# Kernel tuning notes

Hardware: AMD Instinct MI355X
Metric: run time of the kernel (lower is better)

The kernel has to match this reference:

```python
import jax, jax.numpy as jnp
import numpy as np

N = 100_000      # total nodes in batched graph
NE = 800_000     # total edges
G = 1_000        # number of graphs in batch
V_DIM = 128      # node feat dim (== H_DIM, required by GRUCell usage)
E_DIM = 64       # edge feat dim
H_DIM = 128      # hidden dim
K_HEAD = 4       # multi-scale interaction heads


def _leaky(x):
    return jnp.where(x >= 0, x, 0.1 * x)


def _gru_cell(x, h, Wih, Whh, bih, bhh):
    # torch nn.GRUCell math; Wih/Whh stored as [in, 3*h] with (r,z,n) chunk order
    gi = x @ Wih + bih
    gh = h @ Whh + bhh
    ir, iz, inn = jnp.split(gi, 3, axis=-1)
    hr, hz, hn = jnp.split(gh, 3, axis=-1)
    r = jax.nn.sigmoid(ir + hr)
    z = jax.nn.sigmoid(iz + hz)
    n = jnp.tanh(inn + r * hn)
    return (1.0 - z) * n + z * h


def setup_inputs() -> dict:
    key = jax.random.key(0)
    ks = iter(jax.random.split(key, 48))
    def rn(shape, scale=0.05):
        return (jax.random.normal(next(ks), shape) * scale).astype(jnp.float32)
    inp = {}
    inp["v"] = rn((N, V_DIM), 1.0)
    inp["e"] = rn((NE, E_DIM), 1.0)
    inp["s"] = rn((G, V_DIM), 1.0)
    inp["edge_src"] = jax.random.randint(next(ks), (NE,), 0, N)
    inp["edge_dst"] = jax.random.randint(next(ks), (NE,), 0, N)
    inp["node_graph"] = jnp.repeat(jnp.arange(G), N // G)  # sorted segment ids
    # top-level linears (stored [in, out])
    inp["A_w"] = rn((V_DIM, H_DIM)); inp["A_b"] = rn((H_DIM,))
    inp["mA_w"] = rn((K_HEAD, V_DIM, H_DIM)); inp["mA_b"] = rn((K_HEAD, H_DIM))
    inp["mB_w"] = rn((K_HEAD, V_DIM, H_DIM)); inp["mB_b"] = rn((K_HEAD, H_DIM))
    inp["mC_w"] = rn((K_HEAD, H_DIM)); inp["mC_b"] = rn((K_HEAD,))
    inp["mD_w"] = rn((K_HEAD, V_DIM, H_DIM)); inp["mD_b"] = rn((K_HEAD, H_DIM))
    inp["B_w"] = rn((H_DIM * K_HEAD, H_DIM)); inp["B_b"] = rn((H_DIM,))
    inp["C_w"] = rn((V_DIM, H_DIM)); inp["C_b"] = rn((H_DIM,))
    inp["K_w"] = rn((E_DIM, H_DIM)); inp["K_b"] = rn((H_DIM,))
    inp["E_w"] = rn((H_DIM + V_DIM, H_DIM)); inp["E_b"] = rn((H_DIM,))
    for pfx in ("gm", "gs"):
        inp[pfx + "_A_w"] = rn((H_DIM, H_DIM)); inp[pfx + "_A_b"] = rn((H_DIM,))
        inp[pfx + "_B_w"] = rn((H_DIM, H_DIM)); inp[pfx + "_B_b"] = rn((H_DIM,))
        inp[pfx + "_Wih"] = rn((H_DIM, 3 * H_DIM)); inp[pfx + "_Whh"] = rn((H_DIM, 3 * H_DIM))
        inp[pfx + "_bih"] = rn((3 * H_DIM,)); inp[pfx + "_bhh"] = rn((3 * H_DIM,))
    return inp


def reference(v, e, s, edge_src, edge_dst, node_graph,
              A_w, A_b, mA_w, mA_b, mB_w, mB_b, mC_w, mC_b, mD_w, mD_b,
              B_w, B_b, C_w, C_b, K_w, K_b, E_w, E_b,
              gm_A_w, gm_A_b, gm_B_w, gm_B_b, gm_Wih, gm_Whh, gm_bih, gm_bhh,
              gs_A_w, gs_A_b, gs_B_w, gs_B_b, gs_Wih, gs_Whh, gs_bih, gs_bhh):
    # super -> super
    s2s = jnp.tanh(s @ A_w + A_b)                                       # [G,H]
    # multi-head node->super attention pooling (Multi_scale_interaction)
    d_node = jnp.tanh(jnp.einsum('nv,kvh->knh', v, mA_w) + mA_b[:, None, :])     # [K,N,H]
    d_super = jnp.tanh(jnp.einsum('gv,kvh->kgh', s, mB_w) + mB_b[:, None, :])    # [K,G,H]
    a = jnp.einsum('knh,kh->nk', d_node * d_super[:, node_graph, :], mC_w) + mC_b[None, :]  # [N,K]
    a_max = jax.ops.segment_max(a, node_graph, num_segments=G, indices_are_sorted=True)
    a_exp = jnp.exp(a - a_max[node_graph])
    denom = jax.ops.segment_sum(a_exp, node_graph, num_segments=G, indices_are_sorted=True)
    attn = a_exp / denom[node_graph]                                    # per-graph softmax, [N,K]
    d_v = jnp.einsum('nv,kvh->nkh', v, mD_w) + mD_b[None, :, :]         # [N,K,H]
    pooled = jax.ops.segment_sum(d_v * attn[:, :, None], node_graph, num_segments=G,
                                 indices_are_sorted=True)               # [G,K,H]
    m2s = jnp.tanh(pooled.reshape(G, K_HEAD * H_DIM) @ B_w + B_b)       # [G,H]
    # super -> node broadcast
    s2m = jnp.tanh(s @ C_w + C_b)[node_graph]                           # [N,H]
    # edge-wise message: leaky_relu(K(e) * v_src) summed into destination node
    ve = _leaky((e @ K_w + K_b) * v[edge_src])                          # [E,H]
    sve = jax.ops.segment_sum(ve, edge_dst, num_segments=N)             # [N,H]
    m2m = _leaky(jnp.concatenate([sve, v], axis=1) @ E_w + E_b)         # [N,H]
    # adaptive GRU gate: node update
    z_m = jax.nn.sigmoid(m2m @ gm_A_w + gm_A_b + s2m @ gm_B_w + gm_B_b)
    h_m = z_m * s2m + (1.0 - z_m) * m2m
    update_v = _gru_cell(v, h_m, gm_Wih, gm_Whh, gm_bih, gm_bhh)
    # adaptive GRU gate: supernode update
    z_s = jax.nn.sigmoid(s2s @ gs_A_w + gs_A_b + m2s @ gs_B_w + gs_B_b)
    h_s = z_s * m2s + (1.0 - z_s) * s2s
    update_s = _gru_cell(s, h_s, gs_Wih, gs_Whh, gs_bih, gs_bhh)
    return (update_v, update_s)
```

## Files before the change

kernel.cpp:

```cpp
#include <hip/hip_runtime.h>

#define NN   100000
#define NEDG 800000
#define NG   1000
#define HD   128
#define EDIM 64

#define NB3 (NEDG / 64)
#define NB2 ((NN + 63) / 64)
#define NB6 ((NN + 63) / 64)
#define NB4 (NN / 32)
#define W0B 108
#define MH_HIST 3125
#define Z_F4 3200000
#define Z_TOT 3300000
#define ZB ((Z_TOT + 255) / 256)
#define M0_GRID (W0B + NG + ZB)

typedef unsigned short u16;
typedef __bf16 bf16x8 __attribute__((ext_vector_type(8)));
typedef float f32x4 __attribute__((ext_vector_type(4)));
typedef u16 u16x8 __attribute__((ext_vector_type(8)));
typedef unsigned u32x4 __attribute__((ext_vector_type(4)));

#define MFMA16(a, b, c) __builtin_amdgcn_mfma_f32_16x16x32_bf16(a, b, c, 0, 0, 0)

#define WS_E    0
#define WS_GA   4096
#define WS_WIH  6144
#define WS_WHH  12288
#define WS_MA0  18432
#define WS_KW   26624
#define WS_LANES 27648

#define BF(base, NTT, ks, nt, lane) \
    (*(const bf16x8*)(wsw + (size_t)((base) + (((ks) * (NTT) + (nt)) * 64 + (lane))) * 8))

__device__ __forceinline__ float sigmoidf_(float x) { return 1.0f / (1.0f + __expf(-x)); }
__device__ __forceinline__ float tanhf_(float x) {
    float ax = fabsf(x);
    float e  = __expf(-2.0f * ax);
    float t  = (1.0f - e) / (1.0f + e);
    return copysignf(t, x);
}
__device__ __forceinline__ float leaky_(float x) { return x >= 0.f ? x : 0.1f * x; }
__device__ __forceinline__ u16 f2bf(float x) {
    union { float f; unsigned u; } c; c.f = x;
    unsigned r = c.u + 0x7FFF + ((c.u >> 16) & 1);
    return (u16)(r >> 16);
}
__device__ __forceinline__ float bfbits2f(unsigned hw) {
    union { unsigned u; float f; } c; c.u = hw << 16; return c.f;
}
__device__ __forceinline__ unsigned pack2bf(float lo, float hi) {
    return (unsigned)f2bf(lo) | ((unsigned)f2bf(hi) << 16);
}
__device__ __forceinline__ bf16x8 mk8(const float* __restrict__ p) {
    float4 a = *(const float4*)p;
    float4 b = *(const float4*)(p + 4);
    union { u32x4 u; bf16x8 v; } c;
    c.u[0] = pack2bf(a.x, a.y);
    c.u[1] = pack2bf(a.z, a.w);
    c.u[2] = pack2bf(b.x, b.y);
    c.u[3] = pack2bf(b.z, b.w);
    return c.v;
}

__device__ __forceinline__ void stg1(u16* lds, int P, int r, int c, u16 val) {
    int byteoff = (c << 1) ^ ((r & 7) << 4);
    lds[r * P + (byteoff >> 1)] = val;
}
__device__ __forceinline__ bf16x8 ldA(const u16* lds, int P, int r, int ks, int hi) {
    int byteoff = (ks * 64 + (hi << 4)) ^ ((r & 7) << 4);
    return *(const bf16x8*)(lds + r * P + (byteoff >> 1));
}

__device__ __forceinline__ void wconv_body(
    int t,
    const float* __restrict__ E_w, const float* __restrict__ gmA_w,
    const float* __restrict__ Wih, const float* __restrict__ Whh,
    const float* __restrict__ mA_w, const float* __restrict__ K_w,
    u16* __restrict__ dst)
{
    const float* W; int N; int local;
    if (t < 4096)       { W = E_w;  N = 128; local = t; }
    else if (t < 6144)  { W = gmA_w; N = 128; local = t - 4096; }
    else if (t < 12288) { W = Wih;  N = 384; local = t - 6144; }
    else if (t < 18432) { W = Whh;  N = 384; local = t - 12288; }
    else if (t < 26624) { int k = (t - 18432) >> 11; W = mA_w + k * 128 * 128; N = 128; local = (t - 18432) & 2047; }
    else                { W = K_w;  N = 128; local = t - 26624; }
    int lane = local & 63;
    int fid  = local >> 6;
    int NT = N >> 4;
    int ks = fid / NT, nt = fid - ks * NT;
    int krow = ks * 32 + ((lane >> 4) << 3);
    int col  = nt * 16 + (lane & 15);
    u16* d = dst + (size_t)t * 8;
    #pragma unroll
    for (int j = 0; j < 8; j++) d[j] = f2bf(W[(size_t)(krow + j) * N + col]);
}

__device__ __forceinline__ void k1_body(
    int g, int t,
    const float* __restrict__ s,
    const float* __restrict__ A_w, const float* __restrict__ A_b,
    const float* __restrict__ mB_w, const float* __restrict__ mB_b,
    const float* __restrict__ mC_w,
    const float* __restrict__ C_w, const float* __restrict__ C_b,
    const float* __restrict__ gmB_w, const float* __restrict__ gmA_b, const float* __restrict__ gmB_b,
    float* __restrict__ s2s, float* __restrict__ wkg,
    float* __restrict__ s2m_tab, float* __restrict__ t2,
    float* __restrict__ vbar, float* __restrict__ denom)
{
    __shared__ float sm[HD];
    __shared__ float sm2[HD];
    if (t < HD) sm[t] = s[g * HD + t];
    else {
        int i = t - 128;
        #pragma unroll
        for (int j = 0; j < 4; j++) vbar[(size_t)g * 512 + i + 128 * j] = 0.f;
        if (i < 4) denom[g * 4 + i] = 0.f;
    }
    __syncthreads();
    float s2m = 0.f;
    if (t < HD) {
        {
            float a = 0.f;
            #pragma unroll 8
            for (int i = 0; i < HD; i++) a = fmaf(sm[i], A_w[i * HD + t], a);
            s2s[g * HD + t] = tanhf_(a + A_b[t]);
        }
        for (int k = 0; k < 4; k++) {
            float a = 0.f;
            const float* W = mB_w + k * HD * HD;
            #pragma unroll 8
            for (int i = 0; i < HD; i++) a = fmaf(sm[i], W[i * HD + t], a);
            float d = tanhf_(a + mB_b[k * HD + t]);
            wkg[(k * NG + g) * HD + t] = d * mC_w[k * HD + t];
        }
        {
            float a = 0.f;
            #pragma unroll 8
            for (int i = 0; i < HD; i++) a = fmaf(sm[i], C_w[i * HD + t], a);
            s2m = tanhf_(a + C_b[t]);
            s2m_tab[g * HD + t] = s2m;
            sm2[t] = s2m;
        }
    }
    __syncthreads();
    if (t < HD) {
        float a = 0.f;
        #pragma unroll 8
        for (int i = 0; i < HD; i++) a = fmaf(sm2[i], gmB_w[i * HD + t], a);
        t2[g * HD + t] = a + gmA_b[t] + gmB_b[t];
    }
}

__global__ __launch_bounds__(256) void mega0(
    const float* __restrict__ E_w, const float* __restrict__ gmA_w,
    const float* __restrict__ Wih, const float* __restrict__ Whh,
    const float* __restrict__ mA_w, const float* __restrict__ K_w,
    u16* __restrict__ wswz,
    const float* __restrict__ s,
    const float* __restrict__ A_w, const float* __restrict__ A_b,
    const float* __restrict__ mB_w, const float* __restrict__ mB_b,
    const float* __restrict__ mC_w,
    const float* __restrict__ C_w, const float* __restrict__ C_b,
    const float* __restrict__ gmB_w, const float* __restrict__ gmA_b, const float* __restrict__ gmB_b,
    float* __restrict__ s2s, float* __restrict__ wkg,
    float* __restrict__ s2m_tab, float* __restrict__ t2,
    float* __restrict__ vbar, float* __restrict__ denom,
    float* __restrict__ sve, int* __restrict__ cnt)
{
    const int bid = blockIdx.x, tid = threadIdx.x;
    if (bid < W0B) {
        wconv_body(bid * 256 + tid, E_w, gmA_w, Wih, Whh, mA_w, K_w, wswz);
    } else if (bid < W0B + NG) {
        k1_body(bid - W0B, tid, s, A_w, A_b, mB_w, mB_b, mC_w, C_w, C_b,
                gmB_w, gmA_b, gmB_b, s2s, wkg, s2m_tab, t2, vbar, denom);
    } else {
        long idx = (long)(bid - W0B - NG) * 256 + tid;
        if (idx < Z_F4) ((float4*)sve)[idx] = make_float4(0.f, 0.f, 0.f, 0.f);
        else if (idx < Z_TOT) cnt[idx - Z_F4] = 0;
    }
}

__device__ __forceinline__ void k2_body(
    int bid, int tid,
    const float* __restrict__ v, const int* __restrict__ ngr,
    const u16* __restrict__ wsw,
    const float* __restrict__ mA_b, const float* __restrict__ mC_b,
    const float* __restrict__ wkg,
    float* __restrict__ aexp, float* __restrict__ denom)
{
    const int lane = tid & 63, w = tid >> 6;
    const int l15 = lane & 15, hi = lane >> 4;
    const int n0 = bid * 64 + w * 16;
    const int arow = min(n0 + l15, NN - 1);
    bf16x8 av[4];
    #pragma unroll
    for (int ks = 0; ks < 4; ks++)
        av[ks] = mk8(v + (size_t)arow * HD + ks * 32 + hi * 8);
    int gq[4], nodeq[4];
    #pragma unroll
    for (int q = 0; q < 4; q++) {
        int nd = n0 + hi * 4 + q;
        nodeq[q] = nd;
        gq[q] = ngr[min(nd, NN - 1)];
    }
    for (int k = 0; k < 4; k++) {
        float rs[4] = {0.f, 0.f, 0.f, 0.f};
        const float* bias = mA_b + k * HD;
        #pragma unroll
        for (int nt = 0; nt < 8; nt++) {
            f32x4 acc = {0.f, 0.f, 0.f, 0.f};
            #pragma unroll
            for (int ks = 0; ks < 4; ks++)
                acc = MFMA16(av[ks], BF(WS_MA0 + k * 2048, 8, ks, nt, lane), acc);
            int col = nt * 16 + l15;
            float bb = bias[col];
            #pragma unroll
            for (int q = 0; q < 4; q++)
                rs[q] += tanhf_(acc[q] + bb) * wkg[((size_t)k * NG + gq[q]) * HD + col];
        }
        #pragma unroll
        for (int q = 0; q < 4; q++) {
            float x = rs[q];
            x += __shfl_xor(x, 1); x += __shfl_xor(x, 2);
            x += __shfl_xor(x, 4); x += __shfl_xor(x, 8);
            if (l15 == 0 && nodeq[q] < NN) {
                float ev = __expf(x + mC_b[k]);
                aexp[(size_t)nodeq[q] * 4 + k] = ev;
                atomicAdd(&denom[gq[q] * 4 + k], ev);
            }
        }
    }
}

__global__ __launch_bounds__(256) void megaH(
    const int* __restrict__ edst, int* __restrict__ cnt,
    const float* __restrict__ v, const int* __restrict__ ngr,
    const u16* __restrict__ wsw,
    const float* __restrict__ mA_b, const float* __restrict__ mC_b,
    const float* __restrict__ wkg,
    float* __restrict__ aexp, float* __restrict__ denom)
{
    const int bid = blockIdx.x, tid = threadIdx.x;
    if (bid < MH_HIST) {
        int i = bid * 256 + tid;
        if (i < NEDG) atomicAdd(&cnt[edst[i]], 1);
    } else {
        k2_body(bid - MH_HIST, tid, v, ngr, wsw, mA_b, mC_b, wkg, aexp, denom);
    }
}

__global__ __launch_bounds__(256) void k_scan1(const int* __restrict__ cnt,
                                               int* __restrict__ excl, int* __restrict__ bsum) {
    __shared__ int sd[256];
    int t = threadIdx.x, b = blockIdx.x;
    int base = b * 1024 + t * 4;
    int v0 = (base + 0 < NN) ? cnt[base + 0] : 0;
    int v1 = (base + 1 < NN) ? cnt[base + 1] : 0;
    int v2 = (base + 2 < NN) ? cnt[base + 2] : 0;
    int v3 = (base + 3 < NN) ? cnt[base + 3] : 0;
    int s = v0 + v1 + v2 + v3;
    sd[t] = s;
    __syncthreads();
    for (int off = 1; off < 256; off <<= 1) {
        int x = (t >= off) ? sd[t - off] : 0;
        __syncthreads();
        sd[t] += x;
        __syncthreads();
    }
    int incl = sd[t];
    int ex = incl - s;
    if (base + 0 < NN) excl[base + 0] = ex;
    if (base + 1 < NN) excl[base + 1] = ex + v0;
    if (base + 2 < NN) excl[base + 2] = ex + v0 + v1;
    if (base + 3 < NN) excl[base + 3] = ex + v0 + v1 + v2;
    if (t == 255) bsum[b] = incl;
}

#define NSCB 98
__global__ void k_scan2(int* __restrict__ bsum) {
    if (threadIdx.x == 0 && blockIdx.x == 0) {
        int run = 0;
        for (int i = 0; i < NSCB; i++) { int t = bsum[i]; bsum[i] = run; run += t; }
    }
}

__global__ __launch_bounds__(256) void k_scatter_fused(
    const int* __restrict__ edst,
    const int* __restrict__ excl, const int* __restrict__ bsum,
    int* __restrict__ cnt, int* __restrict__ perm)
{
    int i = blockIdx.x * 256 + threadIdx.x;
    if (i < NEDG) {
        int d = edst[i];
        int rank = atomicSub(&cnt[d], 1) - 1;
        perm[excl[d] + bsum[d >> 10] + rank] = i;
    }
}

#define OPW 66
__global__ __launch_bounds__(256) void k3_merge(
    const float* __restrict__ e, const float* __restrict__ v,
    const int* __restrict__ esrc, const int* __restrict__ edst,
    const int* __restrict__ perm,
    const u16* __restrict__ wsw, const float* __restrict__ K_b,
    float* __restrict__ sve)
{
    __shared__ unsigned OUTP[64 * OPW];
    __shared__ int pid[64];
    __shared__ int dsta[64];
    const int tid = threadIdx.x;
    const int e0 = blockIdx.x * 64;
    if (tid < 64) {
        int p = perm[e0 + tid];
        pid[tid] = p;
        dsta[tid] = edst[p];
    }
    const int lane = tid & 63, w = tid >> 6;
    const int l15 = lane & 15, hi = lane >> 4;
    const int rbase = w * 16;
    const int myrow = perm[e0 + rbase + l15];
    bf16x8 ae[2];
    #pragma unroll
    for (int ks = 0; ks < 2; ks++)
        ae[ks] = mk8(e + (size_t)myrow * EDIM + ks * 32 + hi * 8);
    __syncthreads();
    int sq[4];
    #pragma unroll
    for (int q = 0; q < 4; q++) sq[q] = esrc[pid[rbase + hi * 4 + q]];
    u16* OU = (u16*)OUTP;
    #pragma unroll
    for (int nt = 0; nt < 8; nt++) {
        f32x4 acc = {0.f, 0.f, 0.f, 0.f};
        acc = MFMA16(ae[0], BF(WS_KW, 8, 0, nt, lane), acc);
        acc = MFMA16(ae[1], BF(WS_KW, 8, 1, nt, lane), acc);
        int col = nt * 16 + l15;
        float kb = K_b[col];
        #pragma unroll
        for (int q = 0; q < 4; q++) {
            float val = leaky_((acc[q] + kb) * v[(size_t)sq[q] * HD + col]);
            OU[(rbase + hi * 4 + q) * (OPW * 2) + col] = f2bf(val);
        }
    }
    __syncthreads();
    {
        const int cp = tid & 63;
        const int qr = tid >> 6;
        const int r0 = qr * 16;
        int dcur = dsta[r0];
        unsigned x = OUTP[r0 * OPW + cp];
        float a0 = bfbits2f(x & 0xffff), a1 = bfbits2f(x >> 16);
        #pragma unroll
        for (int i = 1; i < 16; i++) {
            int r = r0 + i;
            int d = dsta[r];
            unsigned y = OUTP[r * OPW + cp];
            float y0 = bfbits2f(y & 0xffff), y1 = bfbits2f(y >> 16);
            if (d == dcur) { a0 += y0; a1 += y1; }
            else {
                atomicAdd(&sve[(size_t)dcur * HD + cp * 2 + 0], a0);
                atomicAdd(&sve[(size_t)dcur * HD + cp * 2 + 1], a1);
                dcur = d; a0 = y0; a1 = y1;
            }
        }
        atomicAdd(&sve[(size_t)dcur * HD + cp * 2 + 0], a0);
        atomicAdd(&sve[(size_t)dcur * HD + cp * 2 + 1], a1);
    }
}

__global__ __launch_bounds__(256) void k3_edge_unsorted(
    const float* __restrict__ e, const float* __restrict__ v,
    const int* __restrict__ esrc, const int* __restrict__ edst,
    const u16* __restrict__ wsw, const float* __restrict__ K_b,
    float* __restrict__ sve)
{
    const int tid = threadIdx.x;
    const int e0 = blockIdx.x * 64;
    const int lane = tid & 63, w = tid >> 6;
    const int l15 = lane & 15, hi = lane >> 4;
    const int rbase = w * 16;
    const int myrow = e0 + rbase + l15;
    bf16x8 ae[2];
    #pragma unroll
    for (int ks = 0; ks < 2; ks++)
        ae[ks] = mk8(e + (size_t)myrow * EDIM + ks * 32 + hi * 8);
    int sq[4], dq[4];
    #pragma unroll
    for (int q = 0; q < 4; q++) {
        int ei = e0 + rbase + hi * 4 + q;
        sq[q] = esrc[ei]; dq[q] = edst[ei];
    }
    #pragma unroll
    for (int nt = 0; nt < 8; nt++) {
        f32x4 acc = {0.f, 0.f, 0.f, 0.f};
        acc = MFMA16(ae[0], BF(WS_KW, 8, 0, nt, lane), acc);
        acc = MFMA16(ae[1], BF(WS_KW, 8, 1, nt, lane), acc);
        int col = nt * 16 + l15;
        float kb = K_b[col];
        #pragma unroll
        for (int q = 0; q < 4; q++) {
            float val = leaky_((acc[q] + kb) * v[(size_t)sq[q] * HD + col]);
            atomicAdd(&sve[(size_t)dq[q] * HD + col], val);
        }
    }
}

__device__ __forceinline__ void k4_body(
    int bid, int tid,
    const float* __restrict__ v, const int* __restrict__ ngr,
    const float* __restrict__ aexp, const float* __restrict__ denom,
    float* __restrict__ vbar)
{
    const int d = tid & 127;
    const int hf = tid >> 7;
    const int n0 = bid * 32 + hf * 16;
    int gcur = -1;
    float a0 = 0.f, a1 = 0.f, a2 = 0.f, a3 = 0.f;
    float4 rd = make_float4(0.f, 0.f, 0.f, 0.f);
    for (int nd = 0; nd < 16; nd++) {
        int n = n0 + nd;
        int g = ngr[n];
        if (g != gcur) {
            if (gcur >= 0) {
                atomicAdd(&vbar[(gcur * 4 + 0) * HD + d], a0);
                atomicAdd(&vbar[(gcur * 4 + 1) * HD + d], a1);
                atomicAdd(&vbar[(gcur * 4 + 2) * HD + d], a2);
                atomicAdd(&vbar[(gcur * 4 + 3) * HD + d], a3);
                a0 = a1 = a2 = a3 = 0.f;
            }
            float4 dn = *(const float4*)&denom[g * 4];
            rd = make_float4(1.f / dn.x, 1.f / dn.y, 1.f / dn.z, 1.f / dn.w);
            gcur = g;
        }
        float4 ae = *(const float4*)&aexp[n * 4];
        float vv = v[(size_t)n * HD + d];
        a0 = fmaf(ae.x * rd.x, vv, a0);
        a1 = fmaf(ae.y * rd.y, vv, a1);
        a2 = fmaf(ae.z * rd.z, vv, a2);
        a3 = fmaf(ae.w * rd.w, vv, a3);
    }
    atomicAdd(&vbar[(gcur * 4 + 0) * HD + d], a0);
    atomicAdd(&vbar[(gcur * 4 + 1) * HD + d], a1);
    atomicAdd(&vbar[(gcur * 4 + 2) * HD + d], a2);
    atomicAdd(&vbar[(gcur * 4 + 3) * HD + d], a3);
}

__device__ __forceinline__ void k6_body(
    int bid, int tid, u16* T,
    const float* __restrict__ v, const int* __restrict__ ngr,
    const float* __restrict__ sve, const u16* __restrict__ wsw,
    const float* __restrict__ E_b,
    const float* __restrict__ s2m_tab, const float* __restrict__ t2,
    const float* __restrict__ bih, const float* __restrict__ bhh,
    float* __restrict__ out_v)
{
    const int lane = tid & 63;
    const int l15 = lane & 15, hi = lane >> 4;
    const int n0 = bid * 64 + (tid >> 6) * 16;
    const int arow = min(n0 + l15, NN - 1);
    bf16x8 av[4], ax[4];
    #pragma unroll
    for (int ks = 0; ks < 4; ks++) {
        av[ks] = mk8(v   + (size_t)arow * HD + ks * 32 + hi * 8);
        ax[ks] = mk8(sve + (size_t)arow * HD + ks * 32 + hi * 8);
    }
    int gq[4], nodeq[4];
    #pragma unroll
    for (int q = 0; q < 4; q++) {
        int nd = n0 + hi * 4 + q;
        nodeq[q] = nd;
        gq[q] = ngr[min(nd, NN - 1)];
    }
    unsigned m2mp[8][2];
    #pragma unroll
    for (int nt = 0; nt < 8; nt++) {
        f32x4 acc = {0.f, 0.f, 0.f, 0.f};
        #pragma unroll
        for (int ks = 0; ks < 4; ks++) acc = MFMA16(ax[ks], BF(WS_E, 8, ks, nt, lane), acc);
        #pragma unroll
        for (int ks = 0; ks < 4; ks++) acc = MFMA16(av[ks], BF(WS_E, 8, 4 + ks, nt, lane), acc);
        float eb = E_b[nt * 16 + l15];
        float m0 = leaky_(acc[0] + eb), m1 = leaky_(acc[1] + eb);
        float m2 = leaky_(acc[2] + eb), m3 = leaky_(acc[3] + eb);
        m2mp[nt][0] = pack2bf(m0, m1);
        m2mp[nt][1] = pack2bf(m2, m3);
        int col = nt * 16 + l15;
        stg1(T, 128, hi * 4 + 0, col, (u16)(m2mp[nt][0] & 0xffff));
        stg1(T, 128, hi * 4 + 1, col, (u16)(m2mp[nt][0] >> 16));
        stg1(T, 128, hi * 4 + 2, col, (u16)(m2mp[nt][1] & 0xffff));
        stg1(T, 128, hi * 4 + 3, col, (u16)(m2mp[nt][1] >> 16));
    }
    bf16x8 am[4];
    #pragma unroll
    for (int ks = 0; ks < 4; ks++) am[ks] = ldA(T, 128, l15, ks, hi);
    unsigned hmp[8][2];
    #pragma unroll
    for (int nt = 0; nt < 8; nt++) {
        f32x4 acc = {0.f, 0.f, 0.f, 0.f};
        #pragma unroll
        for (int ks = 0; ks < 4; ks++) acc = MFMA16(am[ks], BF(WS_GA, 8, ks, nt, lane), acc);
        int col = nt * 16 + l15;
        float m2mq[4] = { bfbits2f(m2mp[nt][0] & 0xffff), bfbits2f(m2mp[nt][0] >> 16),
                          bfbits2f(m2mp[nt][1] & 0xffff), bfbits2f(m2mp[nt][1] >> 16) };
        float hm[4];
        #pragma unroll
        for (int q = 0; q < 4; q++) {
            int g = gq[q];
            float z = sigmoidf_(acc[q] + t2[(size_t)g * HD + col]);
            hm[q] = z * s2m_tab[(size_t)g * HD + col] + (1.f - z) * m2mq[q];
        }
        hmp[nt][0] = pack2bf(hm[0], hm[1]);
        hmp[nt][1] = pack2bf(hm[2], hm[3]);
        stg1(T, 128, hi * 4 + 0, col, (u16)(hmp[nt][0] & 0xffff));
        stg1(T, 128, hi * 4 + 1, col, (u16)(hmp[nt][0] >> 16));
        stg1(T, 128, hi * 4 + 2, col, (u16)(hmp[nt][1] & 0xffff));
        stg1(T, 128, hi * 4 + 3, col, (u16)(hmp[nt][1] >> 16));
    }
    bf16x8 ah[4];
    #pragma unroll
    for (int ks = 0; ks < 4; ks++) ah[ks] = ldA(T, 128, l15, ks, hi);
    #pragma unroll
    for (int nt = 0; nt < 8; nt++) {
        f32x4 air = {0.f,0.f,0.f,0.f}, aiz = {0.f,0.f,0.f,0.f}, ain = {0.f,0.f,0.f,0.f};
        f32x4 ahr = {0.f,0.f,0.f,0.f}, ahz = {0.f,0.f,0.f,0.f}, ahn = {0.f,0.f,0.f,0.f};
        #pragma unroll
        for (int ks = 0; ks < 4; ks++) {
            air = MFMA16(av[ks], BF(WS_WIH, 24, ks, nt,      lane), air);
            ahr = MFMA16(ah[ks], BF(WS_WHH, 24, ks, nt,      lane), ahr);
            aiz = MFMA16(av[ks], BF(WS_WIH, 24, ks, nt + 8,  lane), aiz);
            ahz = MFMA16(ah[ks], BF(WS_WHH, 24, ks, nt + 8,  lane), ahz);
            ain = MFMA16(av[ks], BF(WS_WIH, 24, ks, nt + 16, lane), ain);
            ahn = MFMA16(ah[ks], BF(WS_WHH, 24, ks, nt + 16, lane), ahn);
        }
        int col = nt * 16 + l15;
        float br  = bih[col] + bhh[col];
        float bz  = bih[HD + col] + bhh[HD + col];
        float bi3 = bih[2 * HD + col];
        float bh3 = bhh[2 * HD + col];
        float hmq[4] = { bfbits2f(hmp[nt][0] & 0xffff), bfbits2f(hmp[nt][0] >> 16),
                         bfbits2f(hmp[nt][1] & 0xffff), bfbits2f(hmp[nt][1] >> 16) };
        #pragma unroll
        for (int q = 0; q < 4; q++) {
            float r   = sigmoidf_(air[q] + ahr[q] + br);
            float z   = sigmoidf_(aiz[q] + ahz[q] + bz);
            float nnv = tanhf_(ain[q] + bi3 + r * (ahn[q] + bh3));
            if (nodeq[q] < NN)
                out_v[(size_t)nodeq[q] * HD + col] = (1.f - z) * nnv + z * hmq[q];
        }
    }
}

__global__ __launch_bounds__(256) void mega2(
    const float* __restrict__ v, const int* __restrict__ ngr,
    const float* __restrict__ sve, const u16* __restrict__ wsw,
    const float* __restrict__ E_b,
    const float* __restrict__ s2m_tab, const float* __restrict__ t2,
    const float* __restrict__ bih, const float* __restrict__ bhh,
    const float* __restrict__ aexp, const float* __restrict__ denom,
    float* __restrict__ out_v, float* __restrict__ vbar)
{
    __shared__ u16 TT[4][16 * 128];
    const int bid = blockIdx.x, tid = threadIdx.x;
    if (bid < NB6) {
        k6_body(bid, tid, TT[tid >> 6], v, ngr, sve, wsw, E_b, s2m_tab, t2, bih, bhh, out_v);
    } else {
        k4_body(bid - NB6, tid, v, ngr, aexp, denom, vbar);
    }
}

__global__ __launch_bounds__(128) void k5_super(
    const float* __restrict__ s, const float* __restrict__ vbar,
    const float* __restrict__ mD_w, const float* __restrict__ mD_b,
    const float* __restrict__ B_w, const float* __restrict__ B_b,
    const float* __restrict__ s2s,
    const float* __restrict__ gsA_w, const float* __restrict__ gsA_b,
    const float* __restrict__ gsB_w, const float* __restrict__ gsB_b,
    const float* __restrict__ gsWih, const float* __restrict__ gsWhh,
    const float* __restrict__ gsbih, const float* __restrict__ gsbhh,
    float* __restrict__ out_s)
{
    __shared__ float vb[4 * HD];
    __shared__ float p[4 * HD];
    __shared__ float m2s_l[HD];
    __shared__ float s2s_l[HD];
    __shared__ float hs_l[HD];
    __shared__ float srow[HD];
    const int g = blockIdx.x, t = threadIdx.x;
    #pragma unroll
    for (int l = 0; l < 4; l++) vb[t + HD * l] = vbar[(size_t)g * 4 * HD + t + HD * l];
    srow[t]  = s[g * HD + t];
    s2s_l[t] = s2s[g * HD + t];
    __syncthreads();
    for (int k = 0; k < 4; k++) {
        float a = 0.f;
        const float* W = mD_w + k * HD * HD;
        #pragma unroll 8
        for (int i = 0; i < HD; i++) a = fmaf(vb[k * HD + i], W[i * HD + t], a);
        p[k * HD + t] = a + mD_b[k * HD + t];
    }
    __syncthreads();
    float m2s;
    {
        float a = 0.f;
        #pragma unroll 8
        for (int j = 0; j < 4 * HD; j++) a = fmaf(p[j], B_w[j * HD + t], a);
        m2s = tanhf_(a + B_b[t]);
        m2s_l[t] = m2s;
    }
    __syncthreads();
    float hs;
    {
        float za = 0.f, zb = 0.f;
        #pragma unroll 8
        for (int i = 0; i < HD; i++) {
            za = fmaf(s2s_l[i], gsA_w[i * HD + t], za);
            zb = fmaf(m2s_l[i], gsB_w[i * HD + t], zb);
        }
        float z = sigmoidf_(za + gsA_b[t] + zb + gsB_b[t]);
        hs = z * m2s + (1.f - z) * s2s_l[t];
        hs_l[t] = hs;
    }
    __syncthreads();
    float gi0 = 0.f, gh0 = 0.f, gi1 = 0.f, gh1 = 0.f, gi2 = 0.f, gh2 = 0.f;
    #pragma unroll 4
    for (int i = 0; i < HD; i++) {
        float sv = srow[i], hv = hs_l[i];
        gi0 = fmaf(sv, gsWih[i * 384 + t], gi0);
        gh0 = fmaf(hv, gsWhh[i * 384 + t], gh0);
        gi1 = fmaf(sv, gsWih[i * 384 + 128 + t], gi1);
        gh1 = fmaf(hv, gsWhh[i * 384 + 128 + t], gh1);
        gi2 = fmaf(sv, gsWih[i * 384 + 256 + t], gi2);
        gh2 = fmaf(hv, gsWhh[i * 384 + 256 + t], gh2);
    }
    float r  = sigmoidf_(gi0 + gsbih[t] + gh0 + gsbhh[t]);
    float z2 = sigmoidf_(gi1 + gsbih[128 + t] + gh1 + gsbhh[128 + t]);
    float nn = tanhf_(gi2 + gsbih[256 + t] + r * (gh2 + gsbhh[256 + t]));
    out_s[g * HD + t] = (1.f - z2) * nn + z2 * hs;
}

extern "C" void kernel_launch(void* const* d_in, const int* in_sizes, int n_in,
                              void* d_out, int out_size, void* d_ws, size_t ws_size,
                              hipStream_t stream)
{
    const float* v    = (const float*)d_in[0];
    const float* e    = (const float*)d_in[1];
    const float* s    = (const float*)d_in[2];
    const int*   esrc = (const int*)d_in[3];
    const int*   edst = (const int*)d_in[4];
    const int*   ngr  = (const int*)d_in[5];
    const float* A_w  = (const float*)d_in[6];
    const float* A_b  = (const float*)d_in[7];
    const float* mA_w = (const float*)d_in[8];
    const float* mA_b = (const float*)d_in[9];
    const float* mB_w = (const float*)d_in[10];
    const float* mB_b = (const float*)d_in[11];
    const float* mC_w = (const float*)d_in[12];
    const float* mC_b = (const float*)d_in[13];
    const float* mD_w = (const float*)d_in[14];
    const float* mD_b = (const float*)d_in[15];
    const float* B_w  = (const float*)d_in[16];
    const float* B_b  = (const float*)d_in[17];
    const float* C_w  = (const float*)d_in[18];
    const float* C_b  = (const float*)d_in[19];
    const float* K_w  = (const float*)d_in[20];
    const float* K_b  = (const float*)d_in[21];
    const float* E_w  = (const float*)d_in[22];
    const float* E_b  = (const float*)d_in[23];
    const float* gmA_w = (const float*)d_in[24];
    const float* gmA_b = (const float*)d_in[25];
    const float* gmB_w = (const float*)d_in[26];
    const float* gmB_b = (const float*)d_in[27];
    const float* gmWih = (const float*)d_in[28];
    const float* gmWhh = (const float*)d_in[29];
    const float* gmbih = (const float*)d_in[30];
    const float* gmbhh = (const float*)d_in[31];
    const float* gsA_w = (const float*)d_in[32];
    const float* gsA_b = (const float*)d_in[33];
    const float* gsB_w = (const float*)d_in[34];
    const float* gsB_b = (const float*)d_in[35];
    const float* gsWih = (const float*)d_in[36];
    const float* gsWhh = (const float*)d_in[37];
    const float* gsbih = (const float*)d_in[38];
    const float* gsbhh = (const float*)d_in[39];

    float* ws      = (float*)d_ws;
    float* sve     = ws;
    float* aexp    = sve + 12800000;
    float* denom   = aexp + 400000;
    float* wkg     = denom + 4000;
    float* s2s     = wkg + 512000;
    float* s2m_tab = s2s + 128000;
    float* t2      = s2m_tab + 128000;
    float* vbar    = t2 + 128000;
    u16*   wswz    = (u16*)(vbar + 512000);
    int*   isc     = (int*)(wswz + 221184);
    int*   cnt     = isc;
    int*   excl    = cnt + 100000;
    int*   bsum    = excl + 100000;
    int*   startp  = bsum + 128;
    int*   perm    = startp + 100000;
    const size_t NEED_SORT = ((size_t)(perm + 800000 - (int*)d_ws)) * 4;
    const bool do_sort = ws_size >= NEED_SORT;

    float* out_v = (float*)d_out;
    float* out_s = out_v + (size_t)NN * HD;

    mega0<<<M0_GRID, 256, 0, stream>>>(E_w, gmA_w, gmWih, gmWhh, mA_w, K_w, wswz,
                                       s, A_w, A_b, mB_w, mB_b, mC_w, C_w, C_b,
                                       gmB_w, gmA_b, gmB_b, s2s, wkg, s2m_tab, t2,
                                       vbar, denom, sve, cnt);
    megaH<<<MH_HIST + NB2, 256, 0, stream>>>(edst, cnt, v, ngr, wswz, mA_b, mC_b,
                                             wkg, aexp, denom);
    if (do_sort) {
        k_scan1<<<NSCB, 256, 0, stream>>>(cnt, excl, bsum);
        k_scan2<<<1, 64, 0, stream>>>(bsum);
        k_scatter_fused<<<(NEDG + 255) / 256, 256, 0, stream>>>(edst, excl, bsum, cnt, perm);
        k3_merge<<<NB3, 256, 0, stream>>>(e, v, esrc, edst, perm, wswz, K_b, sve);
    } else {
        k3_edge_unsorted<<<NEDG / 64, 256, 0, stream>>>(e, v, esrc, edst, wswz, K_b, sve);
    }
    mega2<<<NB6 + NB4, 256, 0, stream>>>(v, ngr, sve, wswz, E_b, s2m_tab, t2,
                                         gmbih, gmbhh, aexp, denom, out_v, vbar);
    k5_super<<<NG, 128, 0, stream>>>(s, vbar, mD_w, mD_b, B_w, B_b, s2s,
                                     gsA_w, gsA_b, gsB_w, gsB_b,
                                     gsWih, gsWhh, gsbih, gsbhh, out_s);
}
```

Before: 679.7 us.

## Fuse scan passes, co-launch node pooling with edge kernel, merge super update into node kernel

Merges the two scan kernels into one, using an atomic ticket so the last block does the block-sum prefix. Moves the per-graph pooling (k4) out of the node-update kernel and into the same launch as the sorted edge kernel. Folds the supernode GRU kernel into the node-update launch as extra blocks. This removes several launches and lets independent work overlap. The costs are a global-atomic last-block pattern that relies on threadfences, and k5 blocks that now run at 256 threads with half of them idle.

```diff
diff --git a/kernel.cpp b/kernel.cpp
--- a/kernel.cpp
+++ b/kernel.cpp
@@ -13,9 +13,10 @@
 #define W0B 108
 #define MH_HIST 3125
 #define Z_F4 3200000
-#define Z_TOT 3300000
-#define ZB ((Z_TOT + 255) / 256)
+#define Z_EXTRA 100001
+#define ZB ((Z_F4 + Z_EXTRA + 255) / 256)
 #define M0_GRID (W0B + NG + ZB)
+#define NSCB 98
 
 typedef unsigned short u16;
 typedef __bf16 bf16x8 __attribute__((ext_vector_type(8)));
@@ -170,7 +171,7 @@
     float* __restrict__ s2s, float* __restrict__ wkg,
     float* __restrict__ s2m_tab, float* __restrict__ t2,
     float* __restrict__ vbar, float* __restrict__ denom,
-    float* __restrict__ sve, int* __restrict__ cnt)
+    float* __restrict__ sve, int* __restrict__ cnt, int* __restrict__ tick)
 {
     const int bid = blockIdx.x, tid = threadIdx.x;
     if (bid < W0B) {
@@ -181,7 +182,11 @@
     } else {
         long idx = (long)(bid - W0B - NG) * 256 + tid;
         if (idx < Z_F4) ((float4*)sve)[idx] = make_float4(0.f, 0.f, 0.f, 0.f);
-        else if (idx < Z_TOT) cnt[idx - Z_F4] = 0;
+        else {
+            long j = idx - Z_F4;
+            if (j < 100000) cnt[j] = 0;
+            else if (j == 100000) tick[0] = 0;
+        }
     }
 }
 
@@ -254,9 +259,12 @@
     }
 }
 
-__global__ __launch_bounds__(256) void k_scan1(const int* __restrict__ cnt,
-                                               int* __restrict__ excl, int* __restrict__ bsum) {
+__global__ __launch_bounds__(256) void k_scan12(
+    const int* __restrict__ cnt,
+    int* __restrict__ excl, int* __restrict__ bsum, int* __restrict__ tick)
+{
     __shared__ int sd[256];
+    __shared__ int amlast;
     int t = threadIdx.x, b = blockIdx.x;
     int base = b * 1024 + t * 4;
     int v0 = (base + 0 < NN) ? cnt[base + 0] : 0;
@@ -279,13 +287,14 @@
     if (base + 2 < NN) excl[base + 2] = ex + v0 + v1;
     if (base + 3 < NN) excl[base + 3] = ex + v0 + v1 + v2;
     if (t == 255) bsum[b] = incl;
-}
-
-#define NSCB 98
-__global__ void k_scan2(int* __restrict__ bsum) {
-    if (threadIdx.x == 0 && blockIdx.x == 0) {
+    __threadfence();
+    if (t == 0) amlast = (atomicAdd(tick, 1) == NSCB - 1) ? 1 : 0;
+    __syncthreads();
+    if (t == 0 && amlast) {
+        __threadfence();
         int run = 0;
-        for (int i = 0; i < NSCB; i++) { int t = bsum[i]; bsum[i] = run; run += t; }
+        for (int i = 0; i < NSCB; i++) { int tv = bsum[i]; bsum[i] = run; run += tv; }
+        __threadfence();
     }
 }
 
@@ -303,18 +312,18 @@
 }
 
 #define OPW 66
-__global__ __launch_bounds__(256) void k3_merge(
+__device__ __forceinline__ void k3_body(
+    int bid, int tid, char* SM,
     const float* __restrict__ e, const float* __restrict__ v,
     const int* __restrict__ esrc, const int* __restrict__ edst,
     const int* __restrict__ perm,
     const u16* __restrict__ wsw, const float* __restrict__ K_b,
     float* __restrict__ sve)
 {
-    __shared__ unsigned OUTP[64 * OPW];
-    __shared__ int pid[64];
-    __shared__ int dsta[64];
-    const int tid = threadIdx.x;
-    const int e0 = blockIdx.x * 64;
+    unsigned* OUTP = (unsigned*)SM;
+    int* pid  = (int*)(SM + 16896);
+    int* dsta = pid + 64;
+    const int e0 = bid * 64;
     if (tid < 64) {
         int p = perm[e0 + tid];
         pid[tid] = p;
@@ -369,43 +378,6 @@
         }
         atomicAdd(&sve[(size_t)dcur * HD + cp * 2 + 0], a0);
         atomicAdd(&sve[(size_t)dcur * HD + cp * 2 + 1], a1);
-    }
-}
-
-__global__ __launch_bounds__(256) void k3_edge_unsorted(
-    const float* __restrict__ e, const float* __restrict__ v,
-    const int* __restrict__ esrc, const int* __restrict__ edst,
-    const u16* __restrict__ wsw, const float* __restrict__ K_b,
-    float* __restrict__ sve)
-{
-    const int tid = threadIdx.x;
-    const int e0 = blockIdx.x * 64;
-    const int lane = tid & 63, w = tid >> 6;
-    const int l15 = lane & 15, hi = lane >> 4;
-    const int rbase = w * 16;
-    const int myrow = e0 + rbase + l15;
-    bf16x8 ae[2];
-    #pragma unroll
-    for (int ks = 0; ks < 2; ks++)
-        ae[ks] = mk8(e + (size_t)myrow * EDIM + ks * 32 + hi * 8);
-    int sq[4], dq[4];
-    #pragma unroll
-    for (int q = 0; q < 4; q++) {
-        int ei = e0 + rbase + hi * 4 + q;
-        sq[q] = esrc[ei]; dq[q] = edst[ei];
-    }
-    #pragma unroll
-    for (int nt = 0; nt < 8; nt++) {
-        f32x4 acc = {0.f, 0.f, 0.f, 0.f};
-        acc = MFMA16(ae[0], BF(WS_KW, 8, 0, nt, lane), acc);
-        acc = MFMA16(ae[1], BF(WS_KW, 8, 1, nt, lane), acc);
-        int col = nt * 16 + l15;
-        float kb = K_b[col];
-        #pragma unroll
-        for (int q = 0; q < 4; q++) {
-            float val = leaky_((acc[q] + kb) * v[(size_t)sq[q] * HD + col]);
-            atomicAdd(&sve[(size_t)dq[q] * HD + col], val);
-        }
     }
 }
 
@@ -449,6 +421,70 @@
     atomicAdd(&vbar[(gcur * 4 + 3) * HD + d], a3);
 }
 
+__global__ __launch_bounds__(256) void mega3(
+    const float* __restrict__ e, const float* __restrict__ v,
+    const int* __restrict__ esrc, const int* __restrict__ edst,
+    const int* __restrict__ perm,
+    const u16* __restrict__ wsw, const float* __restrict__ K_b,
+    float* __restrict__ sve,
+    const int* __restrict__ ngr,
+    const float* __restrict__ aexp, const float* __restrict__ denom,
+    float* __restrict__ vbar)
+{
+    __shared__ __align__(16) char SM[17408];
+    const int bid = blockIdx.x, tid = threadIdx.x;
+    if (bid < NB3) {
+        k3_body(bid, tid, SM, e, v, esrc, edst, perm, wsw, K_b, sve);
+    } else {
+        k4_body(bid - NB3, tid, v, ngr, aexp, denom, vbar);
+    }
+}
+
+__global__ __launch_bounds__(256) void k3_edge_unsorted(
+    const float* __restrict__ e, const float* __restrict__ v,
+    const int* __restrict__ esrc, const int* __restrict__ edst,
+    const u16* __restrict__ wsw, const float* __restrict__ K_b,
+    float* __restrict__ sve)
+{
+    const int tid = threadIdx.x;
+    const int e0 = blockIdx.x * 64;
+    const int lane = tid & 63, w = tid >> 6;
+    const int l15 = lane & 15, hi = lane >> 4;
+    const int rbase = w * 16;
+    const int myrow = e0 + rbase + l15;
+    bf16x8 ae[2];
+    #pragma unroll
+    for (int ks = 0; ks < 2; ks++)
+        ae[ks] = mk8(e + (size_t)myrow * EDIM + ks * 32 + hi * 8);
+    int sq[4], dq[4];
+    #pragma unroll
+    for (int q = 0; q < 4; q++) {
+        int ei = e0 + rbase + hi * 4 + q;
+        sq[q] = esrc[ei]; dq[q] = edst[ei];
+    }
+    #pragma unroll
+    for (int nt = 0; nt < 8; nt++) {
+        f32x4 acc = {0.f, 0.f, 0.f, 0.f};
+        acc = MFMA16(ae[0], BF(WS_KW, 8, 0, nt, lane), acc);
+        acc = MFMA16(ae[1], BF(WS_KW, 8, 1, nt, lane), acc);
+        int col = nt * 16 + l15;
+        float kb = K_b[col];
+        #pragma unroll
+        for (int q = 0; q < 4; q++) {
+            float val = leaky_((acc[q] + kb) * v[(size_t)sq[q] * HD + col]);
+            atomicAdd(&sve[(size_t)dq[q] * HD + col], val);
+        }
+    }
+}
+
+__global__ __launch_bounds__(256) void k4_standalone(
+    const float* __restrict__ v, const int* __restrict__ ngr,
+    const float* __restrict__ aexp, const float* __restrict__ denom,
+    float* __restrict__ vbar)
+{
+    k4_body(blockIdx.x, threadIdx.x, v, ngr, aexp, denom, vbar);
+}
+
 __device__ __forceinline__ void k6_body(
     int bid, int tid, u16* T,
     const float* __restrict__ v, const int* __restrict__ ngr,
@@ -554,25 +590,8 @@
     }
 }
 
-__global__ __launch_bounds__(256) void mega2(
-    const float* __restrict__ v, const int* __restrict__ ngr,
-    const float* __restrict__ sve, const u16* __restrict__ wsw,
-    const float* __restrict__ E_b,
-    const float* __restrict__ s2m_tab, const float* __restrict__ t2,
-    const float* __restrict__ bih, const float* __restrict__ bhh,
-    const float* __restrict__ aexp, const float* __restrict__ denom,
-    float* __restrict__ out_v, float* __restrict__ vbar)
-{
-    __shared__ u16 TT[4][16 * 128];
-    const int bid = blockIdx.x, tid = threadIdx.x;
-    if (bid < NB6) {
-        k6_body(bid, tid, TT[tid >> 6], v, ngr, sve, wsw, E_b, s2m_tab, t2, bih, bhh, out_v);
-    } else {
-        k4_body(bid - NB6, tid, v, ngr, aexp, denom, vbar);
-    }
-}
-
-__global__ __launch_bounds__(128) void k5_super(
+__device__ __forceinline__ void k5_body(
+    int g, int t, float* SM,
     const float* __restrict__ s, const float* __restrict__ vbar,
     const float* __restrict__ mD_w, const float* __restrict__ mD_b,
     const float* __restrict__ B_w, const float* __restrict__ B_b,
@@ -583,28 +602,32 @@
     const float* __restrict__ gsbih, const float* __restrict__ gsbhh,
     float* __restrict__ out_s)
 {
-    __shared__ float vb[4 * HD];
-    __shared__ float p[4 * HD];
-    __shared__ float m2s_l[HD];
-    __shared__ float s2s_l[HD];
-    __shared__ float hs_l[HD];
-    __shared__ float srow[HD];
-    const int g = blockIdx.x, t = threadIdx.x;
-    #pragma unroll
-    for (int l = 0; l < 4; l++) vb[t + HD * l] = vbar[(size_t)g * 4 * HD + t + HD * l];
-    srow[t]  = s[g * HD + t];
-    s2s_l[t] = s2s[g * HD + t];
-    __syncthreads();
-    for (int k = 0; k < 4; k++) {
-        float a = 0.f;
-        const float* W = mD_w + k * HD * HD;
-        #pragma unroll 8
-        for (int i = 0; i < HD; i++) a = fmaf(vb[k * HD + i], W[i * HD + t], a);
-        p[k * HD + t] = a + mD_b[k * HD + t];
-    }
-    __syncthreads();
-    float m2s;
-    {
+    float* vb    = SM;
+    float* p     = SM + 512;
+    float* m2s_l = SM + 1024;
+    float* s2s_l = SM + 1152;
+    float* hs_l  = SM + 1280;
+    float* srow  = SM + 1408;
+    const bool act = t < HD;
+    if (act) {
+        #pragma unroll
+        for (int l = 0; l < 4; l++) vb[t + HD * l] = vbar[(size_t)g * 4 * HD + t + HD * l];
+        srow[t]  = s[g * HD + t];
+        s2s_l[t] = s2s[g * HD + t];
+    }
+    __syncthreads();
+    if (act) {
+        for (int k = 0; k < 4; k++) {
+            float a = 0.f;
+            const float* W = mD_w + k * HD * HD;
+            #pragma unroll 8
+            for (int i = 0; i < HD; i++) a = fmaf(vb[k * HD + i], W[i * HD + t], a);
+            p[k * HD + t] = a + mD_b[k * HD + t];
+        }
+    }
+    __syncthreads();
+    float m2s = 0.f;
+    if (act) {
         float a = 0.f;
         #pragma unroll 8
         for (int j = 0; j < 4 * HD; j++) a = fmaf(p[j], B_w[j * HD + t], a);
@@ -612,8 +635,8 @@
         m2s_l[t] = m2s;
     }
     __syncthreads();
-    float hs;
-    {
+    float hs = 0.f;
+    if (act) {
         float za = 0.f, zb = 0.f;
         #pragma unroll 8
         for (int i = 0; i < HD; i++) {
@@ -625,21 +648,51 @@
         hs_l[t] = hs;
     }
     __syncthreads();
-    float gi0 = 0.f, gh0 = 0.f, gi1 = 0.f, gh1 = 0.f, gi2 = 0.f, gh2 = 0.f;
-    #pragma unroll 4
-    for (int i = 0; i < HD; i++) {
-        float sv = srow[i], hv = hs_l[i];
-        gi0 = fmaf(sv, gsWih[i * 384 + t], gi0);
-        gh0 = fmaf(hv, gsWhh[i * 384 + t], gh0);
-        gi1 = fmaf(sv, gsWih[i * 384 + 128 + t], gi1);
-        gh1 = fmaf(hv, gsWhh[i * 384 + 128 + t], gh1);
-        gi2 = fmaf(sv, gsWih[i * 384 + 256 + t], gi2);
-        gh2 = fmaf(hv, gsWhh[i * 384 + 256 + t], gh2);
-    }
-    float r  = sigmoidf_(gi0 + gsbih[t] + gh0 + gsbhh[t]);
-    float z2 = sigmoidf_(gi1 + gsbih[128 + t] + gh1 + gsbhh[128 + t]);
-    float nn = tanhf_(gi2 + gsbih[256 + t] + r * (gh2 + gsbhh[256 + t]));
-    out_s[g * HD + t] = (1.f - z2) * nn + z2 * hs;
+    if (act) {
+        float gi0 = 0.f, gh0 = 0.f, gi1 = 0.f, gh1 = 0.f, gi2 = 0.f, gh2 = 0.f;
+        #pragma unroll 4
+        for (int i = 0; i < HD; i++) {
+            float sv = srow[i], hv = hs_l[i];
+            gi0 = fmaf(sv, gsWih[i * 384 + t], gi0);
+            gh0 = fmaf(hv, gsWhh[i * 384 + t], gh0);
+            gi1 = fmaf(sv, gsWih[i * 384 + 128 + t], gi1);
+            gh1 = fmaf(hv, gsWhh[i * 384 + 128 + t], gh1);
+            gi2 = fmaf(sv, gsWih[i * 384 + 256 + t], gi2);
+            gh2 = fmaf(hv, gsWhh[i * 384 + 256 + t], gh2);
+        }
+        float r  = sigmoidf_(gi0 + gsbih[t] + gh0 + gsbhh[t]);
+        float z2 = sigmoidf_(gi1 + gsbih[128 + t] + gh1 + gsbhh[128 + t]);
+        float nn = tanhf_(gi2 + gsbih[256 + t] + r * (gh2 + gsbhh[256 + t]));
+        out_s[g * HD + t] = (1.f - z2) * nn + z2 * hs;
+    }
+}
+
+__global__ __launch_bounds__(256) void mega2b(
+    const float* __restrict__ v, const int* __restrict__ ngr,
+    const float* __restrict__ sve, const u16* __restrict__ wsw,
+    const float* __restrict__ E_b,
+    const float* __restrict__ s2m_tab, const float* __restrict__ t2,
+    const float* __restrict__ bih, const float* __restrict__ bhh,
+    float* __restrict__ out_v,
+    const float* __restrict__ s, const float* __restrict__ vbar,
+    const float* __restrict__ mD_w, const float* __restrict__ mD_b,
+    const float* __restrict__ B_w, const float* __restrict__ B_b,
+    const float* __restrict__ s2s,
+    const float* __restrict__ gsA_w, const float* __restrict__ gsA_b,
+    const float* __restrict__ gsB_w, const float* __restrict__ gsB_b,
+    const float* __restrict__ gsWih, const float* __restrict__ gsWhh,
+    const float* __restrict__ gsbih, const float* __restrict__ gsbhh,
+    float* __restrict__ out_s)
+{
+    __shared__ __align__(16) char SM[16384];
+    const int bid = blockIdx.x, tid = threadIdx.x;
+    if (bid < NB6) {
+        k6_body(bid, tid, (u16*)(SM + (tid >> 6) * 4096), v, ngr, sve, wsw,
+                E_b, s2m_tab, t2, bih, bhh, out_v);
+    } else {
+        k5_body(bid - NB6, tid, (float*)SM, s, vbar, mD_w, mD_b, B_w, B_b, s2s,
+                gsA_w, gsA_b, gsB_w, gsB_b, gsWih, gsWhh, gsbih, gsbhh, out_s);
+    }
 }
 
 extern "C" void kernel_launch(void* const* d_in, const int* in_sizes, int n_in,
@@ -701,8 +754,8 @@
     int*   cnt     = isc;
     int*   excl    = cnt + 100000;
     int*   bsum    = excl + 100000;
-    int*   startp  = bsum + 128;
-    int*   perm    = startp + 100000;
+    int*   tick    = bsum + 128;
+    int*   perm    = tick + 100000;
     const size_t NEED_SORT = ((size_t)(perm + 800000 - (int*)d_ws)) * 4;
     const bool do_sort = ws_size >= NEED_SORT;
 
@@ -712,20 +765,21 @@
     mega0<<<M0_GRID, 256, 0, stream>>>(E_w, gmA_w, gmWih, gmWhh, mA_w, K_w, wswz,
                                        s, A_w, A_b, mB_w, mB_b, mC_w, C_w, C_b,
                                        gmB_w, gmA_b, gmB_b, s2s, wkg, s2m_tab, t2,
-                                       vbar, denom, sve, cnt);
+                                       vbar, denom, sve, cnt, tick);
     megaH<<<MH_HIST + NB2, 256, 0, stream>>>(edst, cnt, v, ngr, wswz, mA_b, mC_b,
                                              wkg, aexp, denom);
     if (do_sort) {
-        k_scan1<<<NSCB, 256, 0, stream>>>(cnt, excl, bsum);
-        k_scan2<<<1, 64, 0, stream>>>(bsum);
+        k_scan12<<<NSCB, 256, 0, stream>>>(cnt, excl, bsum, tick);
         k_scatter_fused<<<(NEDG + 255) / 256, 256, 0, stream>>>(edst, excl, bsum, cnt, perm);
-        k3_merge<<<NB3, 256, 0, stream>>>(e, v, esrc, edst, perm, wswz, K_b, sve);
+        mega3<<<NB3 + NB4, 256, 0, stream>>>(e, v, esrc, edst, perm, wswz, K_b, sve,
+                                             ngr, aexp, denom, vbar);
     } else {
         k3_edge_unsorted<<<NEDG / 64, 256, 0, stream>>>(e, v, esrc, edst, wswz, K_b, sve);
-    }
-    mega2<<<NB6 + NB4, 256, 0, stream>>>(v, ngr, sve, wswz, E_b, s2m_tab, t2,
-                                         gmbih, gmbhh, aexp, denom, out_v, vbar);
-    k5_super<<<NG, 128, 0, stream>>>(s, vbar, mD_w, mD_b, B_w, B_b, s2s,
-                                     gsA_w, gsA_b, gsB_w, gsB_b,
-                                     gsWih, gsWhh, gsbih, gsbhh, out_s);
-}
+        k4_standalone<<<NB4, 256, 0, stream>>>(v, ngr, aexp, denom, vbar);
+    }
+    mega2b<<<NB6 + NG, 256, 0, stream>>>(v, ngr, sve, wswz, E_b, s2m_tab, t2,
+                                         gmbih, gmbhh, out_v,
+                                         s, vbar, mD_w, mD_b, B_w, B_b, s2s,
+                                         gsA_w, gsA_b, gsB_w, gsB_b,
+                                         gsWih, gsWhh, gsbih, gsbhh, out_s);
+}
```

Measured after the change: 715.0 us. +5.2%, slower.
